# Kernel tuning notes

Measured on AMD Instinct MI355X. Metric: run time of the kernel, lower is better.

The kernel has to match this reference:

```python
import jax, jax.numpy as jnp
import numpy as np

B, N, DIN, D, PHI, RHO, L = 4096, 10, 32, 128, 256, 128, 3
EPS = 1e-5


def setup_inputs() -> dict:
    key = jax.random.key(0)
    ks = jax.random.split(key, 24)
    def p(k, shape):
        return jax.random.normal(k, shape, jnp.float32) * 0.05
    return {
        "A": jax.random.normal(ks[0], (B, N, N), jnp.float32),
        "X": jax.random.normal(ks[1], (B, N, DIN), jnp.float32),
        "home_mask": jax.random.randint(ks[2], (B, N), 0, 2).astype(jnp.int32),
        "We1": p(ks[3], (DIN, D)), "be1": p(ks[4], (D,)),
        "We2": p(ks[5], (D, D)), "be2": p(ks[6], (D,)),
        "rgcn_w": p(ks[7], (L, 2, D, D)),      # per-relation weights
        "rgcn_root": p(ks[8], (L, D, D)),       # root (self) weight
        "rgcn_b": p(ks[9], (L, D)),
        "l1w": p(ks[10], (L, D, D)), "l1b": p(ks[11], (L, D)),
        "l2w": p(ks[12], (L, D, D)), "l2b": p(ks[13], (L, D)),
        "ln_g": jnp.ones((D,), jnp.float32), "ln_b": jnp.zeros((D,), jnp.float32),
        "p1w": p(ks[14], (D, PHI)), "p1b": p(ks[15], (PHI,)),
        "p2w": p(ks[16], (PHI, PHI)), "p2b": p(ks[17], (PHI,)),
        "r1w": p(ks[18], (PHI, RHO)), "r1b": p(ks[19], (RHO,)),
        "r2w": p(ks[20], (RHO, 1)), "r2b": p(ks[21], (1,)),
    }


def _layernorm(x, g, b):
    mu = x.mean(-1, keepdims=True)
    var = ((x - mu) ** 2).mean(-1, keepdims=True)
    return (x - mu) / jnp.sqrt(var + EPS) * g + b


def reference(A, X, home_mask, We1, be1, We2, be2, rgcn_w, rgcn_root, rgcn_b,
              l1w, l1b, l2w, l2b, ln_g, ln_b, p1w, p1b, p2w, p2b,
              r1w, r1b, r2w, r2b):
    BN = B * N
    hm = home_mask.astype(jnp.float32)
    am = 1.0 - hm
    # embedders (dropout layers are identity in eval)
    H = jax.nn.relu(X @ We1 + be1)
    H = (H @ We2 + be2).reshape(BN, D)
    # A ~ randn is nonzero everywhere -> edge list = all (b,i,j) pairs,
    # in the same row-major order torch.nonzero produces.
    bidx = jnp.repeat(jnp.arange(BN), N)          # b*N+i for each edge (row)
    row = bidx
    col = (jnp.repeat(jnp.arange(B), N * N) * N + jnp.tile(jnp.arange(N), BN))
    ew = A.reshape(-1)                             # edge weight
    aw = jnp.abs(ew)
    m1 = (ew > 0).astype(jnp.float32)              # relation 1 mask
    m0 = 1.0 - m1                                  # relation 0 mask
    agg = jnp.zeros_like(H)
    for l in range(L):
        H = H + agg
        # RGCNConv (mean aggregation per relation + root + bias)
        xj = H[row]                                # [E, D] gather of sources
        s0 = jax.ops.segment_sum(xj * m0[:, None], col, num_segments=BN)
        s1 = jax.ops.segment_sum(xj * m1[:, None], col, num_segments=BN)
        c0 = jax.ops.segment_sum(m0, col, num_segments=BN)
        c1 = jax.ops.segment_sum(m1, col, num_segments=BN)
        mean0 = s0 / jnp.maximum(c0, 1.0)[:, None]
        mean1 = s1 / jnp.maximum(c1, 1.0)[:, None]
        H2 = mean0 @ rgcn_w[l, 0] + mean1 @ rgcn_w[l, 1] + H @ rgcn_root[l] + rgcn_b[l]
        # outer gather-scale-scatter
        msg = H2[col] * aw[:, None]                # [E, D]
        agg = jax.ops.segment_sum(msg, row, num_segments=BN)
        agg = jax.nn.relu(_layernorm(agg, ln_g, ln_b))
        # Linear -> ReLU -> (Dropout=id) -> Linear
        agg = jax.nn.relu(agg @ l1w[l] + l1b[l])
        agg = agg @ l2w[l] + l2b[l]
    H = (H + agg).reshape(B, N, D)
    # DeepSet phi (dropout = identity)
    phi = jax.nn.relu(H @ p1w + p1b)
    phi = jax.nn.relu(phi @ p2w + p2b)             # [B, N, PHI]
    hs = (phi * hm[..., None]).sum(axis=1)
    aws = (phi * am[..., None]).sum(axis=1)
    def rho(s):
        return (jax.nn.relu(s @ r1w + r1b) @ r2w + r2b)[..., 0]
    return 0.5 + 0.5 * jnp.tanh(rho(hs) - rho(aws))
```

## Files before the change

kernel.cpp:

```cpp
#include <hip/hip_runtime.h>
#include <hip/hip_bf16.h>
#include <math.h>

#define B_    4096
#define N_    10
#define DIN_  32
#define D_    128
#define PHI_  256
#define RHO_  128
#define L_    3
#define EPS_  1e-5f

__device__ __forceinline__ short f2bs(float f) {
    unsigned u = __float_as_uint(f);
    u += 0x7fffu + ((u >> 16) & 1u);
    return (short)(u >> 16);
}
__device__ __forceinline__ float bs2f(short s) {
    return __uint_as_float(((unsigned)(unsigned short)s) << 16);
}
__device__ __forceinline__ short2 f2bs2(float x, float y) {
    float2 f; f.x = x; f.y = y;
    __hip_bfloat162 h = __float22bfloat162_rn(f);
    short2 r;
    __builtin_memcpy(&r, &h, 4);
    return r;
}

typedef short bf16x8 __attribute__((ext_vector_type(8)));
typedef float f32x4  __attribute__((ext_vector_type(4)));
typedef float v2f    __attribute__((ext_vector_type(2)));

__device__ __forceinline__ v2f splat2(float s) { v2f r; r.x = s; r.y = s; return r; }
__device__ __forceinline__ v2f fma2(v2f a, v2f b, v2f c) { return __builtin_elementwise_fma(a, b, c); }

#define WS_WE1 0
#define WS_WE2 4096
#define WS_RGW 20480
#define WS_RGR 118784
#define WS_L1  167936
#define WS_L2  217088
#define WS_P1  266240
#define WS_P2  299008
#define WS_R1  364544

__global__ __launch_bounds__(64)
void prep_weights(const float* __restrict__ We1, const float* __restrict__ We2,
                  const float* __restrict__ rgw, const float* __restrict__ rgr,
                  const float* __restrict__ l1w, const float* __restrict__ l2w,
                  const float* __restrict__ p1w, const float* __restrict__ p2w,
                  const float* __restrict__ r1w, short* __restrict__ ws)
{
    int bi = blockIdx.x, l = threadIdx.x;
    const float* src; int KS, Nw, dstOff, tt;
    if      (bi <   8) { src = We1; KS = 1; Nw = 128; dstOff = WS_WE1; tt = bi; }
    else if (bi <  40) { src = We2; KS = 4; Nw = 128; dstOff = WS_WE2; tt = bi - 8; }
    else if (bi < 232) { int m = (bi - 40) >> 5;  src = rgw + m * 16384; KS = 4; Nw = 128; dstOff = WS_RGW + m * 16384; tt = (bi - 40)  & 31; }
    else if (bi < 328) { int m = (bi - 232) >> 5; src = rgr + m * 16384; KS = 4; Nw = 128; dstOff = WS_RGR + m * 16384; tt = (bi - 232) & 31; }
    else if (bi < 424) { int m = (bi - 328) >> 5; src = l1w + m * 16384; KS = 4; Nw = 128; dstOff = WS_L1  + m * 16384; tt = (bi - 328) & 31; }
    else if (bi < 520) { int m = (bi - 424) >> 5; src = l2w + m * 16384; KS = 4; Nw = 128; dstOff = WS_L2  + m * 16384; tt = (bi - 424) & 31; }
    else if (bi < 584) { src = p1w; KS = 4; Nw = 256; dstOff = WS_P1; tt = bi - 520; }
    else if (bi < 712) { src = p2w; KS = 8; Nw = 256; dstOff = WS_P2; tt = bi - 584; }
    else               { src = r1w; KS = 8; Nw = 128; dstOff = WS_R1; tt = bi - 712; }
    int nt = tt / KS, ks = tt - nt * KS;
    int kbase = ks * 32 + (l >> 4) * 8;
    int col   = nt * 16 + (l & 15);
    union { short s[8]; int4 v; } u;
#pragma unroll
    for (int j = 0; j < 8; ++j)
        u.s[j] = f2bs(src[(size_t)(kbase + j) * Nw + col]);
    *(int4*)(ws + dstOff + ((size_t)tt * 64 + l) * 8) = u.v;
}


template<int NT>
__device__ __forceinline__ void initC(f32x4* acc, const float* __restrict__ bias, int c16) {
#pragma unroll
    for (int nt = 0; nt < NT; ++nt) {
        float bv = bias[nt * 16 + c16];
        acc[nt] = (f32x4){bv, bv, bv, bv};
    }
}

template<int KS, int NT>
__device__ __forceinline__ void mm_a16(const short* __restrict__ Wf, const short* __restrict__ Ab,
                                       int ldA, int mrow, int q, int lane, f32x4* acc) {
#pragma unroll
    for (int ks = 0; ks < KS; ++ks) {
        bf16x8 a = *(const bf16x8*)(Ab + mrow * ldA + ks * 32 + q * 8);
#pragma unroll
        for (int nt = 0; nt < NT; ++nt) {
            bf16x8 bv = *(const bf16x8*)(Wf + ((size_t)(nt * KS + ks) * 64 + lane) * 8);
            acc[nt] = __builtin_amdgcn_mfma_f32_16x16x32_bf16(a, bv, acc[nt], 0, 0, 0);
        }
    }
}

template<int KS, int NT>
__device__ __forceinline__ void mm_a32(const short* __restrict__ Wf, const float* __restrict__ Af,
                                       int ldA, int mrow, int q, int lane, f32x4* acc) {
#pragma unroll
    for (int ks = 0; ks < KS; ++ks) {
        const float* p = Af + mrow * ldA + ks * 32 + q * 8;
        f32x4 x0 = *(const f32x4*)p;
        f32x4 x1 = *(const f32x4*)(p + 4);
        union { short2 p2[4]; bf16x8 v; } a;
        a.p2[0] = f2bs2(x0[0], x0[1]); a.p2[1] = f2bs2(x0[2], x0[3]);
        a.p2[2] = f2bs2(x1[0], x1[1]); a.p2[3] = f2bs2(x1[2], x1[3]);
#pragma unroll
        for (int nt = 0; nt < NT; ++nt) {
            bf16x8 bv = *(const bf16x8*)(Wf + ((size_t)(nt * KS + ks) * 64 + lane) * 8);
            acc[nt] = __builtin_amdgcn_mfma_f32_16x16x32_bf16(a.v, bv, acc[nt], 0, 0, 0);
        }
    }
}

template<int KS>
__device__ __forceinline__ void mm8p_a16(const short* __restrict__ Wf,
                                         const short* __restrict__ Ab, int ldA,
                                         int mrow, int q, int lane, f32x4* acc)
{
    const short* ap = Ab + mrow * ldA + q * 8;
    const short* wp = Wf + lane * 8;
    bf16x8 acur = *(const bf16x8*)ap;
    bf16x8 bcur[8], bnxt[8];
#pragma unroll
    for (int nt = 0; nt < 8; ++nt) bcur[nt] = *(const bf16x8*)(wp + (size_t)nt * KS * 512);
#pragma unroll
    for (int ks = 0; ks < KS; ++ks) {
        bf16x8 anxt = acur;
#pragma unroll
        for (int nt = 0; nt < 8; ++nt) bnxt[nt] = bcur[nt];
        if (ks + 1 < KS) {
            anxt = *(const bf16x8*)(ap + (ks + 1) * 32);
#pragma unroll
            for (int nt = 0; nt < 8; ++nt)
                bnxt[nt] = *(const bf16x8*)(wp + (size_t)(nt * KS + ks + 1) * 512);
        }
#pragma unroll
        for (int nt = 0; nt < 8; ++nt)
            acc[nt] = __builtin_amdgcn_mfma_f32_16x16x32_bf16(acur, bcur[nt], acc[nt], 0, 0, 0);
        acur = anxt;
#pragma unroll
        for (int nt = 0; nt < 8; ++nt) bcur[nt] = bnxt[nt];
    }
}

template<int KS>
__device__ __forceinline__ void mm8p_a32(const short* __restrict__ Wf,
                                         const float* __restrict__ Af, int ldA,
                                         int mrow, int q, int lane, f32x4* acc)
{
    const float* ap = Af + mrow * ldA + q * 8;
    const short* wp = Wf + lane * 8;
    auto cvt = [](const float* p) {
        f32x4 x0 = *(const f32x4*)p;
        f32x4 x1 = *(const f32x4*)(p + 4);
        union { short2 p2[4]; bf16x8 v; } a;
        a.p2[0] = f2bs2(x0[0], x0[1]); a.p2[1] = f2bs2(x0[2], x0[3]);
        a.p2[2] = f2bs2(x1[0], x1[1]); a.p2[3] = f2bs2(x1[2], x1[3]);
        return a.v;
    };
    bf16x8 acur = cvt(ap);
    bf16x8 bcur[8], bnxt[8];
#pragma unroll
    for (int nt = 0; nt < 8; ++nt) bcur[nt] = *(const bf16x8*)(wp + (size_t)nt * KS * 512);
#pragma unroll
    for (int ks = 0; ks < KS; ++ks) {
        bf16x8 anxt = acur;
#pragma unroll
        for (int nt = 0; nt < 8; ++nt) bnxt[nt] = bcur[nt];
        if (ks + 1 < KS) {
            anxt = cvt(ap + (ks + 1) * 32);
#pragma unroll
            for (int nt = 0; nt < 8; ++nt)
                bnxt[nt] = *(const bf16x8*)(wp + (size_t)(nt * KS + ks + 1) * 512);
        }
#pragma unroll
        for (int nt = 0; nt < 8; ++nt)
            acc[nt] = __builtin_amdgcn_mfma_f32_16x16x32_bf16(acur, bcur[nt], acc[nt], 0, 0, 0);
        acur = anxt;
#pragma unroll
        for (int nt = 0; nt < 8; ++nt) bcur[nt] = bnxt[nt];
    }
}

template<int NT, bool RELU>
__device__ __forceinline__ void storeC16(const f32x4* acc, short* __restrict__ dst,
                                         int ldD, int q, int c16) {
#pragma unroll
    for (int nt = 0; nt < NT; ++nt) {
#pragma unroll
        for (int i = 0; i < 4; ++i) {
            int r = q * 4 + i;
            if (r < 10) {
                float v = acc[nt][i];
                if (RELU) v = fmaxf(v, 0.f);
                dst[r * ldD + nt * 16 + c16] = f2bs(v);
            }
        }
    }
}

#define HLD  132
#define GLD  264
#define H2LD 136

__global__ __launch_bounds__(256, 2)
void gcn_main(const float* __restrict__ A, const float* __restrict__ X,
              const int* __restrict__ home_mask,
              const float* __restrict__ be1, const float* __restrict__ be2,
              const float* __restrict__ rgcn_b,
              const float* __restrict__ l1b, const float* __restrict__ l2b,
              const float* __restrict__ ln_g, const float* __restrict__ ln_b,
              const float* __restrict__ p1b, const float* __restrict__ p2b,
              const float* __restrict__ r1b, const float* __restrict__ r2w,
              const short* __restrict__ ws, float* __restrict__ out)
{
    const int t    = threadIdx.x;
    const int w    = t >> 6;
    const int lane = t & 63;
    const int q    = lane >> 4;
    const int c16  = lane & 15;
    const int mrow = (c16 < 10) ? c16 : 9;
    const int b    = blockIdx.x * 4 + w;

    __shared__ __align__(16) float HfS[4][N_ * HLD];
    __shared__ __align__(16) short GbS[4][N_ * GLD];
    __shared__ __align__(16) short H2S[4][N_ * H2LD];
    __shared__ float AabsS[4][100], M1S[4][100];
    __shared__ float invc0S[4][N_], invc1S[4][N_];
    __shared__ float hmfS[4][16], awfS[4][16];

    short* S0   = &GbS[w][0];
    short* S1   = &GbS[w][136];
    short* RhoS = &H2S[w][0];

    {
        const float* Ab = A + (size_t)b * 100;
#pragma unroll
        for (int e = lane; e < 100; e += 64) {
            float a = Ab[e];
            AabsS[w][e] = fabsf(a);
            M1S[w][e]  = (a > 0.f) ? 1.f : 0.f;
        }
        if (lane < 16) {
            float hm = 0.f, aw = 0.f;
            if (lane < 10) { hm = (float)home_mask[b * N_ + lane]; aw = 1.f - hm; }
            hmfS[w][lane] = hm; awfS[w][lane] = aw;
        }
        if (lane < 10) {
            float c1 = 0.f;
#pragma unroll
            for (int i = 0; i < 10; ++i) c1 += M1S[w][i * 10 + lane];
            invc1S[w][lane] = 1.f / fmaxf(c1, 1.f);
            invc0S[w][lane] = 1.f / fmaxf(10.f - c1, 1.f);
        }
    }

    __syncthreads();
    {
        f32x4 acc[8];
        initC<8>(acc, be1, c16);
        const float* xg = X + (size_t)b * (N_ * DIN_) + mrow * DIN_ + q * 8;
        f32x4 x0 = *(const f32x4*)xg;
        f32x4 x1 = *(const f32x4*)(xg + 4);
        union { short2 p2[4]; bf16x8 v; } a;
        a.p2[0] = f2bs2(x0[0], x0[1]); a.p2[1] = f2bs2(x0[2], x0[3]);
        a.p2[2] = f2bs2(x1[0], x1[1]); a.p2[3] = f2bs2(x1[2], x1[3]);
#pragma unroll
        for (int nt = 0; nt < 8; ++nt) {
            bf16x8 bv = *(const bf16x8*)(ws + WS_WE1 + ((size_t)nt * 64 + lane) * 8);
            acc[nt] = __builtin_amdgcn_mfma_f32_16x16x32_bf16(a.v, bv, acc[nt], 0, 0, 0);
        }
        storeC16<8, true>(acc, S0, GLD, q, c16);
    }
    __syncthreads();
    {
        f32x4 acc[8];
        initC<8>(acc, be2, c16);
        mm8p_a16<4>(ws + WS_WE2, S0, GLD, mrow, q, lane, acc);
#pragma unroll
        for (int nt = 0; nt < 8; ++nt)
#pragma unroll
            for (int i = 0; i < 4; ++i) {
                int r = q * 4 + i;
                if (r < 10) HfS[w][r * HLD + nt * 16 + c16] = acc[nt][i];
            }
    }

    const v2f lg2 = *(const v2f*)(ln_g + 2 * lane);
    const v2f lb2 = *(const v2f*)(ln_b + 2 * lane);

    for (int ll = 0; ll < L_; ++ll) {
        {
            v2f hv[N_];
#pragma unroll
            for (int i = 0; i < N_; ++i) hv[i] = *(const v2f*)(&HfS[w][i * HLD] + 2 * lane);
            v2f st = hv[0];
#pragma unroll
            for (int i = 1; i < N_; ++i) st += hv[i];
#pragma unroll
            for (int j = 0; j < N_; ++j) {
                v2f s1 = splat2(0.f);
#pragma unroll
                for (int i = 0; i < N_; ++i) s1 = fma2(splat2(M1S[w][i * 10 + j]), hv[i], s1);
                v2f m0 = (st - s1) * splat2(invc0S[w][j]);
                v2f m1 = s1 * splat2(invc1S[w][j]);
                *(short2*)(S0 + j * GLD + 2 * lane) = f2bs2(m0.x, m0.y);
                *(short2*)(S1 + j * GLD + 2 * lane) = f2bs2(m1.x, m1.y);
            }
        }
        __syncthreads();
        {
            f32x4 acc[8];
            initC<8>(acc, rgcn_b + ll * D_, c16);
            mm8p_a16<4>(ws + WS_RGW + (size_t)(ll * 2 + 0) * 16384, S0, GLD, mrow, q, lane, acc);
            mm8p_a16<4>(ws + WS_RGW + (size_t)(ll * 2 + 1) * 16384, S1, GLD, mrow, q, lane, acc);
            mm8p_a32<4>(ws + WS_RGR + (size_t)ll * 16384, &HfS[w][0], HLD, mrow, q, lane, acc);
            storeC16<8, false>(acc, &H2S[w][0], H2LD, q, c16);
        }
        {
            v2f ag[N_];
#pragma unroll
            for (int i = 0; i < N_; ++i) ag[i] = splat2(0.f);
#pragma unroll
            for (int j = 0; j < N_; ++j) {
                short2 hh = *(const short2*)(&H2S[w][j * H2LD] + 2 * lane);
                v2f h2; h2.x = bs2f(hh.x); h2.y = bs2f(hh.y);
#pragma unroll
                for (int i = 0; i < N_; ++i)
                    ag[i] = fma2(splat2(AabsS[w][i * 10 + j]), h2, ag[i]);
            }
#pragma unroll
            for (int i = 0; i < N_; ++i) {
                float s  = ag[i].x + ag[i].y;
                float ss = fmaf(ag[i].x, ag[i].x, ag[i].y * ag[i].y);
#pragma unroll
                for (int off = 32; off > 0; off >>= 1) {
                    s  += __shfl_xor(s,  off);
                    ss += __shfl_xor(ss, off);
                }
                float mu   = s * (1.f / 128.f);
                float var  = ss * (1.f / 128.f) - mu * mu;
                float rstd = rsqrtf(var + EPS_);
                v2f v = fma2((ag[i] - splat2(mu)) * splat2(rstd), lg2, lb2);
                *(short2*)(S0 + i * GLD + 2 * lane) = f2bs2(fmaxf(v.x, 0.f), fmaxf(v.y, 0.f));
            }
        }
        __syncthreads();
        {
            f32x4 acc[8];
            initC<8>(acc, l1b + ll * D_, c16);
            mm8p_a16<4>(ws + WS_L1 + (size_t)ll * 16384, S0, GLD, mrow, q, lane, acc);
            storeC16<8, true>(acc, S1, GLD, q, c16);
        }
        __syncthreads();
        {
            f32x4 acc[8];
            initC<8>(acc, l2b + ll * D_, c16);
            mm8p_a16<4>(ws + WS_L2 + (size_t)ll * 16384, S1, GLD, mrow, q, lane, acc);
#pragma unroll
            for (int nt = 0; nt < 8; ++nt)
#pragma unroll
                for (int i = 0; i < 4; ++i) {
                    int r = q * 4 + i;
                    if (r < 10) HfS[w][r * HLD + nt * 16 + c16] += acc[nt][i];
                }
        }
    }

    __syncthreads();
    {
        f32x4 acc[16];
        initC<16>(acc, p1b, c16);
        mm_a32<4, 16>(ws + WS_P1, &HfS[w][0], HLD, mrow, q, lane, acc);
        storeC16<16, true>(acc, &GbS[w][0], GLD, q, c16);
    }
    __syncthreads();
    {
        f32x4 acc[16];
        initC<16>(acc, p2b, c16);
        mm_a16<8, 16>(ws + WS_P2, &GbS[w][0], GLD, mrow, q, lane, acc);
        float hm0 = hmfS[w][q * 4 + 0], hm1 = hmfS[w][q * 4 + 1];
        float hm2 = hmfS[w][q * 4 + 2], hm3 = hmfS[w][q * 4 + 3];
        float aw0 = awfS[w][q * 4 + 0], aw1 = awfS[w][q * 4 + 1];
        float aw2 = awfS[w][q * 4 + 2], aw3 = awfS[w][q * 4 + 3];
#pragma unroll
        for (int tt = 0; tt < 16; ++tt) {
            float v0 = fmaxf(acc[tt][0], 0.f), v1 = fmaxf(acc[tt][1], 0.f);
            float v2 = fmaxf(acc[tt][2], 0.f), v3 = fmaxf(acc[tt][3], 0.f);
            float hp = hm0 * v0 + hm1 * v1 + hm2 * v2 + hm3 * v3;
            float ap = aw0 * v0 + aw1 * v1 + aw2 * v2 + aw3 * v3;
            hp += __shfl_xor(hp, 16); hp += __shfl_xor(hp, 32);
            ap += __shfl_xor(ap, 16); ap += __shfl_xor(ap, 32);
            if (lane < 16) {
                RhoS[tt * 16 + lane]       = f2bs(hp);
                RhoS[256 + tt * 16 + lane] = f2bs(ap);
            }
        }
    }
    __syncthreads();
    {
        f32x4 acc[8];
        initC<8>(acc, r1b, c16);
        const int rr = (c16 < 2) ? c16 : 0;
        mm_a16<8, 8>(ws + WS_R1, RhoS, 256, rr, q, lane, acc);
        float d = 0.f;
        if (q == 0) {
#pragma unroll
            for (int tt = 0; tt < 8; ++tt) {
                float vh = fmaxf(acc[tt][0], 0.f);
                float va = fmaxf(acc[tt][1], 0.f);
                d = fmaf(vh - va, r2w[tt * 16 + c16], d);
            }
        }
#pragma unroll
        for (int off = 32; off > 0; off >>= 1) d += __shfl_xor(d, off);
        if (lane == 0) out[b] = 0.5f + 0.5f * tanhf(d);
    }
}

extern "C" void kernel_launch(void* const* d_in, const int* in_sizes, int n_in,
                              void* d_out, int out_size, void* d_ws, size_t ws_size,
                              hipStream_t stream) {
    const float* A         = (const float*)d_in[0];
    const float* X         = (const float*)d_in[1];
    const int*   home_mask = (const int*)  d_in[2];
    const float* We1       = (const float*)d_in[3];
    const float* be1       = (const float*)d_in[4];
    const float* We2       = (const float*)d_in[5];
    const float* be2       = (const float*)d_in[6];
    const float* rgcn_w    = (const float*)d_in[7];
    const float* rgcn_root = (const float*)d_in[8];
    const float* rgcn_b    = (const float*)d_in[9];
    const float* l1w       = (const float*)d_in[10];
    const float* l1b       = (const float*)d_in[11];
    const float* l2w       = (const float*)d_in[12];
    const float* l2b       = (const float*)d_in[13];
    const float* ln_g      = (const float*)d_in[14];
    const float* ln_b      = (const float*)d_in[15];
    const float* p1w       = (const float*)d_in[16];
    const float* p1b       = (const float*)d_in[17];
    const float* p2w       = (const float*)d_in[18];
    const float* p2b       = (const float*)d_in[19];
    const float* r1w       = (const float*)d_in[20];
    const float* r1b       = (const float*)d_in[21];
    const float* r2w       = (const float*)d_in[22];

    short* ws = (short*)d_ws;

    prep_weights<<<776, 64, 0, stream>>>(We1, We2, rgcn_w, rgcn_root,
                                         l1w, l2w, p1w, p2w, r1w, ws);
    gcn_main<<<B_ / 4, 256, 0, stream>>>(A, X, home_mask, be1, be2, rgcn_b,
                                         l1b, l2b, ln_g, ln_b, p1b, p2b,
                                         r1b, r2w, ws, (float*)d_out);
}
```

Baseline: 260.9 us.

## Stage weight fragments into LDS via global_load_lds shared across waves

```diff
diff --git a/kernel.cpp b/kernel.cpp
--- a/kernel.cpp
+++ b/kernel.cpp
@@ -73,6 +73,23 @@
 }
 
 
+__device__ __forceinline__ void stage16(const short* g, short* l) {
+    __builtin_amdgcn_global_load_lds(
+        (const __attribute__((address_space(1))) void*)g,
+        (__attribute__((address_space(3))) void*)l, 16, 0, 0);
+}
+
+template<int NF>
+__device__ __forceinline__ void stageW(const short* __restrict__ src,
+                                       short* __restrict__ dst, int w, int lane) {
+    constexpr int PER = NF / 4;
+#pragma unroll
+    for (int k = 0; k < PER; ++k) {
+        int f = w * PER + k;
+        stage16(src + (size_t)f * 512 + lane * 8, dst + f * 512);
+    }
+}
+
 template<int NT>
 __device__ __forceinline__ void initC(f32x4* acc, const float* __restrict__ bias, int c16) {
 #pragma unroll
@@ -82,106 +99,62 @@
     }
 }
 
-template<int KS, int NT>
-__device__ __forceinline__ void mm_a16(const short* __restrict__ Wf, const short* __restrict__ Ab,
-                                       int ldA, int mrow, int q, int lane, f32x4* acc) {
-#pragma unroll
-    for (int ks = 0; ks < KS; ++ks) {
-        bf16x8 a = *(const bf16x8*)(Ab + mrow * ldA + ks * 32 + q * 8);
-#pragma unroll
-        for (int nt = 0; nt < NT; ++nt) {
-            bf16x8 bv = *(const bf16x8*)(Wf + ((size_t)(nt * KS + ks) * 64 + lane) * 8);
-            acc[nt] = __builtin_amdgcn_mfma_f32_16x16x32_bf16(a, bv, acc[nt], 0, 0, 0);
-        }
-    }
-}
-
-template<int KS, int NT>
-__device__ __forceinline__ void mm_a32(const short* __restrict__ Wf, const float* __restrict__ Af,
-                                       int ldA, int mrow, int q, int lane, f32x4* acc) {
-#pragma unroll
-    for (int ks = 0; ks < KS; ++ks) {
-        const float* p = Af + mrow * ldA + ks * 32 + q * 8;
-        f32x4 x0 = *(const f32x4*)p;
-        f32x4 x1 = *(const f32x4*)(p + 4);
-        union { short2 p2[4]; bf16x8 v; } a;
-        a.p2[0] = f2bs2(x0[0], x0[1]); a.p2[1] = f2bs2(x0[2], x0[3]);
-        a.p2[2] = f2bs2(x1[0], x1[1]); a.p2[3] = f2bs2(x1[2], x1[3]);
-#pragma unroll
-        for (int nt = 0; nt < NT; ++nt) {
-            bf16x8 bv = *(const bf16x8*)(Wf + ((size_t)(nt * KS + ks) * 64 + lane) * 8);
-            acc[nt] = __builtin_amdgcn_mfma_f32_16x16x32_bf16(a.v, bv, acc[nt], 0, 0, 0);
-        }
-    }
-}
-
-template<int KS>
-__device__ __forceinline__ void mm8p_a16(const short* __restrict__ Wf,
-                                         const short* __restrict__ Ab, int ldA,
-                                         int mrow, int q, int lane, f32x4* acc)
+template<int KS, int NTtot>
+__device__ __forceinline__ void mmStaged16(const short* __restrict__ wsrc,
+                                           const short* __restrict__ Ab, int ldA,
+                                           int mrow, int q, int lane, int w,
+                                           short* __restrict__ Wst, f32x4* acc)
 {
-    const short* ap = Ab + mrow * ldA + q * 8;
-    const short* wp = Wf + lane * 8;
-    bf16x8 acur = *(const bf16x8*)ap;
-    bf16x8 bcur[8], bnxt[8];
-#pragma unroll
-    for (int nt = 0; nt < 8; ++nt) bcur[nt] = *(const bf16x8*)(wp + (size_t)nt * KS * 512);
-#pragma unroll
-    for (int ks = 0; ks < KS; ++ks) {
-        bf16x8 anxt = acur;
-#pragma unroll
-        for (int nt = 0; nt < 8; ++nt) bnxt[nt] = bcur[nt];
-        if (ks + 1 < KS) {
-            anxt = *(const bf16x8*)(ap + (ks + 1) * 32);
-#pragma unroll
-            for (int nt = 0; nt < 8; ++nt)
-                bnxt[nt] = *(const bf16x8*)(wp + (size_t)(nt * KS + ks + 1) * 512);
-        }
-#pragma unroll
-        for (int nt = 0; nt < 8; ++nt)
-            acc[nt] = __builtin_amdgcn_mfma_f32_16x16x32_bf16(acur, bcur[nt], acc[nt], 0, 0, 0);
-        acur = anxt;
-#pragma unroll
-        for (int nt = 0; nt < 8; ++nt) bcur[nt] = bnxt[nt];
-    }
-}
-
-template<int KS>
-__device__ __forceinline__ void mm8p_a32(const short* __restrict__ Wf,
-                                         const float* __restrict__ Af, int ldA,
-                                         int mrow, int q, int lane, f32x4* acc)
+    constexpr int NTC = ((16 / KS) < NTtot) ? (16 / KS) : NTtot;
+    constexpr int NF  = NTC * KS;
+    constexpr int NCH = NTtot / NTC;
+#pragma unroll
+    for (int c = 0; c < NCH; ++c) {
+        stageW<NF>(wsrc + (size_t)c * NF * 512, Wst, w, lane);
+        __syncthreads();
+#pragma unroll
+        for (int ks = 0; ks < KS; ++ks) {
+            bf16x8 a = *(const bf16x8*)(Ab + mrow * ldA + ks * 32 + q * 8);
+#pragma unroll
+            for (int nt = 0; nt < NTC; ++nt) {
+                bf16x8 bv = *(const bf16x8*)(Wst + ((nt * KS + ks) * 64 + lane) * 8);
+                acc[c * NTC + nt] =
+                    __builtin_amdgcn_mfma_f32_16x16x32_bf16(a, bv, acc[c * NTC + nt], 0, 0, 0);
+            }
+        }
+        __syncthreads();
+    }
+}
+
+template<int KS, int NTtot>
+__device__ __forceinline__ void mmStaged32(const short* __restrict__ wsrc,
+                                           const float* __restrict__ Af, int ldA,
+                                           int mrow, int q, int lane, int w,
+                                           short* __restrict__ Wst, f32x4* acc)
 {
-    const float* ap = Af + mrow * ldA + q * 8;
-    const short* wp = Wf + lane * 8;
-    auto cvt = [](const float* p) {
-        f32x4 x0 = *(const f32x4*)p;
-        f32x4 x1 = *(const f32x4*)(p + 4);
-        union { short2 p2[4]; bf16x8 v; } a;
-        a.p2[0] = f2bs2(x0[0], x0[1]); a.p2[1] = f2bs2(x0[2], x0[3]);
-        a.p2[2] = f2bs2(x1[0], x1[1]); a.p2[3] = f2bs2(x1[2], x1[3]);
-        return a.v;
-    };
-    bf16x8 acur = cvt(ap);
-    bf16x8 bcur[8], bnxt[8];
-#pragma unroll
-    for (int nt = 0; nt < 8; ++nt) bcur[nt] = *(const bf16x8*)(wp + (size_t)nt * KS * 512);
-#pragma unroll
-    for (int ks = 0; ks < KS; ++ks) {
-        bf16x8 anxt = acur;
-#pragma unroll
-        for (int nt = 0; nt < 8; ++nt) bnxt[nt] = bcur[nt];
-        if (ks + 1 < KS) {
-            anxt = cvt(ap + (ks + 1) * 32);
-#pragma unroll
-            for (int nt = 0; nt < 8; ++nt)
-                bnxt[nt] = *(const bf16x8*)(wp + (size_t)(nt * KS + ks + 1) * 512);
-        }
-#pragma unroll
-        for (int nt = 0; nt < 8; ++nt)
-            acc[nt] = __builtin_amdgcn_mfma_f32_16x16x32_bf16(acur, bcur[nt], acc[nt], 0, 0, 0);
-        acur = anxt;
-#pragma unroll
-        for (int nt = 0; nt < 8; ++nt) bcur[nt] = bnxt[nt];
+    constexpr int NTC = ((16 / KS) < NTtot) ? (16 / KS) : NTtot;
+    constexpr int NF  = NTC * KS;
+    constexpr int NCH = NTtot / NTC;
+#pragma unroll
+    for (int c = 0; c < NCH; ++c) {
+        stageW<NF>(wsrc + (size_t)c * NF * 512, Wst, w, lane);
+        __syncthreads();
+#pragma unroll
+        for (int ks = 0; ks < KS; ++ks) {
+            const float* p = Af + mrow * ldA + ks * 32 + q * 8;
+            f32x4 x0 = *(const f32x4*)p;
+            f32x4 x1 = *(const f32x4*)(p + 4);
+            union { short2 p2[4]; bf16x8 v; } a;
+            a.p2[0] = f2bs2(x0[0], x0[1]); a.p2[1] = f2bs2(x0[2], x0[3]);
+            a.p2[2] = f2bs2(x1[0], x1[1]); a.p2[3] = f2bs2(x1[2], x1[3]);
+#pragma unroll
+            for (int nt = 0; nt < NTC; ++nt) {
+                bf16x8 bv = *(const bf16x8*)(Wst + ((nt * KS + ks) * 64 + lane) * 8);
+                acc[c * NTC + nt] =
+                    __builtin_amdgcn_mfma_f32_16x16x32_bf16(a.v, bv, acc[c * NTC + nt], 0, 0, 0);
+            }
+        }
+        __syncthreads();
     }
 }
 
@@ -228,6 +201,7 @@
     __shared__ __align__(16) float HfS[4][N_ * HLD];
     __shared__ __align__(16) short GbS[4][N_ * GLD];
     __shared__ __align__(16) short H2S[4][N_ * H2LD];
+    __shared__ __align__(16) short WstS[16 * 512];
     __shared__ float AabsS[4][100], M1S[4][100];
     __shared__ float invc0S[4][N_], invc1S[4][N_];
     __shared__ float hmfS[4][16], awfS[4][16];
@@ -258,6 +232,7 @@
         }
     }
 
+    stageW<8>(ws + WS_WE1, WstS, w, lane);
     __syncthreads();
     {
         f32x4 acc[8];
@@ -270,7 +245,7 @@
         a.p2[2] = f2bs2(x1[0], x1[1]); a.p2[3] = f2bs2(x1[2], x1[3]);
 #pragma unroll
         for (int nt = 0; nt < 8; ++nt) {
-            bf16x8 bv = *(const bf16x8*)(ws + WS_WE1 + ((size_t)nt * 64 + lane) * 8);
+            bf16x8 bv = *(const bf16x8*)(WstS + (nt * 64 + lane) * 8);
             acc[nt] = __builtin_amdgcn_mfma_f32_16x16x32_bf16(a.v, bv, acc[nt], 0, 0, 0);
         }
         storeC16<8, true>(acc, S0, GLD, q, c16);
@@ -279,7 +254,7 @@
     {
         f32x4 acc[8];
         initC<8>(acc, be2, c16);
-        mm8p_a16<4>(ws + WS_WE2, S0, GLD, mrow, q, lane, acc);
+        mmStaged16<4, 8>(ws + WS_WE2, S0, GLD, mrow, q, lane, w, WstS, acc);
 #pragma unroll
         for (int nt = 0; nt < 8; ++nt)
 #pragma unroll
@@ -311,13 +286,12 @@
                 *(short2*)(S1 + j * GLD + 2 * lane) = f2bs2(m1.x, m1.y);
             }
         }
-        __syncthreads();
         {
             f32x4 acc[8];
             initC<8>(acc, rgcn_b + ll * D_, c16);
-            mm8p_a16<4>(ws + WS_RGW + (size_t)(ll * 2 + 0) * 16384, S0, GLD, mrow, q, lane, acc);
-            mm8p_a16<4>(ws + WS_RGW + (size_t)(ll * 2 + 1) * 16384, S1, GLD, mrow, q, lane, acc);
-            mm8p_a32<4>(ws + WS_RGR + (size_t)ll * 16384, &HfS[w][0], HLD, mrow, q, lane, acc);
+            mmStaged16<4, 8>(ws + WS_RGW + (size_t)(ll * 2 + 0) * 16384, S0, GLD, mrow, q, lane, w, WstS, acc);
+            mmStaged16<4, 8>(ws + WS_RGW + (size_t)(ll * 2 + 1) * 16384, S1, GLD, mrow, q, lane, w, WstS, acc);
+            mmStaged32<4, 8>(ws + WS_RGR + (size_t)ll * 16384, &HfS[w][0], HLD, mrow, q, lane, w, WstS, acc);
             storeC16<8, false>(acc, &H2S[w][0], H2LD, q, c16);
         }
         {
@@ -348,18 +322,16 @@
                 *(short2*)(S0 + i * GLD + 2 * lane) = f2bs2(fmaxf(v.x, 0.f), fmaxf(v.y, 0.f));
             }
         }
-        __syncthreads();
         {
             f32x4 acc[8];
             initC<8>(acc, l1b + ll * D_, c16);
-            mm8p_a16<4>(ws + WS_L1 + (size_t)ll * 16384, S0, GLD, mrow, q, lane, acc);
+            mmStaged16<4, 8>(ws + WS_L1 + (size_t)ll * 16384, S0, GLD, mrow, q, lane, w, WstS, acc);
             storeC16<8, true>(acc, S1, GLD, q, c16);
         }
-        __syncthreads();
         {
             f32x4 acc[8];
             initC<8>(acc, l2b + ll * D_, c16);
-            mm8p_a16<4>(ws + WS_L2 + (size_t)ll * 16384, S1, GLD, mrow, q, lane, acc);
+            mmStaged16<4, 8>(ws + WS_L2 + (size_t)ll * 16384, S1, GLD, mrow, q, lane, w, WstS, acc);
 #pragma unroll
             for (int nt = 0; nt < 8; ++nt)
 #pragma unroll
@@ -370,18 +342,16 @@
         }
     }
 
-    __syncthreads();
     {
         f32x4 acc[16];
         initC<16>(acc, p1b, c16);
-        mm_a32<4, 16>(ws + WS_P1, &HfS[w][0], HLD, mrow, q, lane, acc);
+        mmStaged32<4, 16>(ws + WS_P1, &HfS[w][0], HLD, mrow, q, lane, w, WstS, acc);
         storeC16<16, true>(acc, &GbS[w][0], GLD, q, c16);
     }
-    __syncthreads();
     {
         f32x4 acc[16];
         initC<16>(acc, p2b, c16);
-        mm_a16<8, 16>(ws + WS_P2, &GbS[w][0], GLD, mrow, q, lane, acc);
+        mmStaged16<8, 16>(ws + WS_P2, &GbS[w][0], GLD, mrow, q, lane, w, WstS, acc);
         float hm0 = hmfS[w][q * 4 + 0], hm1 = hmfS[w][q * 4 + 1];
         float hm2 = hmfS[w][q * 4 + 2], hm3 = hmfS[w][q * 4 + 3];
         float aw0 = awfS[w][q * 4 + 0], aw1 = awfS[w][q * 4 + 1];
@@ -400,12 +370,11 @@
             }
         }
     }
-    __syncthreads();
     {
         f32x4 acc[8];
         initC<8>(acc, r1b, c16);
         const int rr = (c16 < 2) ? c16 : 0;
-        mm_a16<8, 8>(ws + WS_R1, RhoS, 256, rr, q, lane, acc);
+        mmStaged16<8, 8>(ws + WS_R1, RhoS, 256, rr, q, lane, w, WstS, acc);
         float d = 0.f;
         if (q == 0) {
 #pragma unroll
```

Result: faster. 253.8 us (-2.7%).
